# Kernel tuning notes

Hardware: AMD Instinct MI355X
Metric: run time of the kernel (lower is better)

## Reference

```python
import jax, jax.numpy as jnp
from jax import lax
import numpy as np

N_QUBITS = 8


def _apply_1q(state, w, n, m00, m01, m10, m11):
    # state: (B, 2, 2, ..., 2); wire w lives on axis 1+w (wire 0 = most significant)
    st = jnp.moveaxis(state, 1 + w, -1)
    a0, a1 = st[..., 0], st[..., 1]
    b0 = m00 * a0 + m01 * a1
    b1 = m10 * a0 + m11 * a1
    st = jnp.stack([b0, b1], axis=-1)
    return jnp.moveaxis(st, -1, 1 + w)


def _apply_rx(state, theta, w, n):
    # RX(t) = [[cos t/2, -i sin t/2], [-i sin t/2, cos t/2]], per-batch theta
    shp = (-1,) + (1,) * (n - 1)
    c = jnp.cos(theta / 2).reshape(shp).astype(jnp.complex64)
    s = (-1j) * jnp.sin(theta / 2).reshape(shp).astype(jnp.complex64)
    return _apply_1q(state, w, n, c, s, s, c)


def _apply_rz(state, theta, w, n):
    # RZ(t) = diag(e^{-it/2}, e^{+it/2})
    shp = (-1,) + (1,) * (n - 1)
    e = jnp.exp(-0.5j * theta.astype(jnp.complex64)).reshape(shp)
    return _apply_1q(state, w, n, e, jnp.zeros_like(e), jnp.zeros_like(e), jnp.conj(e))


def _apply_cnot(state, ctrl, tgt, n):
    st = jnp.moveaxis(state, (1 + ctrl, 1 + tgt), (-2, -1))
    st = jnp.stack([st[..., 0, :], st[..., 1, ::-1]], axis=-2)
    return jnp.moveaxis(st, (-2, -1), (1 + ctrl, 1 + tgt))


def _circuit_probs(params):
    # params: (B, n). Simulate the fixed PennyLane circuit: for each wire w:
    # RX(params[w]) on w, RZ(params[(w+1)%n]) on w, CNOT(w, (w+1)%n).
    B, n = params.shape
    state = jnp.zeros((B, 2 ** n), jnp.complex64).at[:, 0].set(1.0)
    state = state.reshape((B,) + (2,) * n)
    for w in range(n):
        state = _apply_rx(state, params[:, w], w, n)
        state = _apply_rz(state, params[:, (w + 1) % n], w, n)
        state = _apply_cnot(state, w, (w + 1) % n, n)
    probs = jnp.abs(state.reshape(B, -1)) ** 2  # (B, 2^n), wire 0 most significant
    p = probs[:, :n]
    return p / jnp.sum(p, axis=1, keepdims=True)


def _qgate(W, b, x):
    params = x @ W.T + b  # (B, n_qubits)
    return _circuit_probs(params)


def setup_inputs() -> dict:
    key = jax.random.key(0)
    ks = jax.random.split(key, 9)
    S, B, D, N = 1024, 128, 256, N_QUBITS
    fan_in = D + N
    lim = 1.0 / np.sqrt(fan_in)
    u = lambda k, shape: jax.random.uniform(k, shape, jnp.float32, -lim, lim)
    return {
        "inputs": jax.random.normal(ks[0], (S, B, D), jnp.float32),
        "Wf": u(ks[1], (N, fan_in)), "bf": u(ks[2], (N,)),
        "Wi": u(ks[3], (N, fan_in)), "bi": u(ks[4], (N,)),
        "Wu": u(ks[5], (N, fan_in)), "bu": u(ks[6], (N,)),
        "Wo": u(ks[7], (N, fan_in)), "bo": u(ks[8], (N,)),
    }


def reference(inputs, Wf, bf, Wi, bi, Wu, bu, Wo, bo):
    S, B, D = inputs.shape
    N = Wf.shape[0]  # hidden_dim == n_qubits
    h0 = jnp.zeros((B, N), inputs.dtype)
    c0 = jnp.zeros((B, N), inputs.dtype)

    def step(carry, x):
        h, c = carry
        comb = jnp.concatenate([x, h], axis=1)  # (B, D+N)
        f = _qgate(Wf, bf, comb)
        i = _qgate(Wi, bi, comb)
        g = jnp.tanh(_qgate(Wu, bu, comb))
        o = _qgate(Wo, bo, comb)
        c_new = f * c + i * g
        h_new = o * jnp.tanh(c_new)
        return (h_new, c_new), h_new

    (h_n, c_n), outputs = lax.scan(step, (h0, c0), inputs)
    return outputs, h_n, c_n
```

## Files before the change

kernel.cpp:

```cpp
#include <hip/hip_runtime.h>

#define S_STEPS 1024
#define BATCH 128
#define NQ 8
#define XW_FLOATS (BATCH * 32 * 1024)

using v2f     = float __attribute__((ext_vector_type(2)));
using frag_ab = __attribute__((ext_vector_type(8))) short;
using frag_cd = __attribute__((ext_vector_type(4))) float;

#define INV2PI 0.15915494309189535f

template<int CTRL>
__device__ __forceinline__ float dppf(float x) {
  return __int_as_float(__builtin_amdgcn_update_dpp(0, __float_as_int(x), CTRL, 0xf, 0xf, true));
}
__device__ __forceinline__ float bperm(int addr, float v) {
  return __int_as_float(__builtin_amdgcn_ds_bpermute(addr, __float_as_int(v)));
}
__device__ __forceinline__ short f2bf(float f) {
  unsigned u = __float_as_uint(f);
  return (short)((u + 0x7FFFu + ((u >> 16) & 1u)) >> 16);
}
__device__ __forceinline__ float bf2f(short h) {
  return __uint_as_float(((unsigned)(unsigned short)h) << 16);
}

__global__ __launch_bounds__(512) void qlstm_pre(
    const float* __restrict__ x,
    const float* __restrict__ Wf, const float* __restrict__ bf_,
    const float* __restrict__ Wi, const float* __restrict__ bi,
    const float* __restrict__ Wu, const float* __restrict__ bu,
    const float* __restrict__ Wo, const float* __restrict__ bo,
    float* __restrict__ xw)
{
  __shared__ short whi[32 * 264];
  __shared__ short wlo[32 * 264];

  const int tid = threadIdx.x;

  {
    const int base = tid * 16;
    const int c = base >> 8, k0 = base & 255;
    const int g = c >> 3, w = c & 7;
    const float* Wg = (g == 0) ? Wf : (g == 1) ? Wi : (g == 2) ? Wu : Wo;
    const float* p = Wg + w * 264 + k0;
    const int o = c * 264 + k0;
#pragma unroll
    for (int q = 0; q < 2; ++q) {
      float4 va = *(const float4*)(p + q * 8);
      float4 vb = *(const float4*)(p + q * 8 + 4);
      float vv[8] = {va.x, va.y, va.z, va.w, vb.x, vb.y, vb.z, vb.w};
      frag_ab h8, l8;
#pragma unroll
      for (int j = 0; j < 8; ++j) {
        float wv = vv[j] * INV2PI;
        short h = f2bf(wv);
        h8[j] = h;
        l8[j] = f2bf(wv - bf2f(h));
      }
      *(frag_ab*)&whi[o + q * 8] = h8;
      *(frag_ab*)&wlo[o + q * 8] = l8;
    }
  }
  __syncthreads();

  const int lane = tid & 63;
  const int m  = lane & 15;
  const int kg = lane >> 4;
  const int gid = blockIdx.x * 8 + (tid >> 6);
  const int b  = gid >> 6;
  const int t0 = (gid & 63) << 4;

  float bb[2][4];
#pragma unroll
  for (int n = 0; n < 2; ++n)
#pragma unroll
    for (int r = 0; r < 4; ++r) {
      int c = n * 16 + kg * 4 + r;
      int g = c >> 3, w = c & 7;
      const float* bg = (g == 0) ? bf_ : (g == 1) ? bi : (g == 2) ? bu : bo;
      bb[n][r] = bg[w] * INV2PI;
    }

  const float* xbase = x + ((size_t)(t0 + m) * 128 + b) * 256 + kg * 8;
  const int w0 = m * 264 + kg * 8;
  const int w1 = w0 + 16 * 264;

  frag_cd acc0 = {0.f, 0.f, 0.f, 0.f};
  frag_cd acc1 = {0.f, 0.f, 0.f, 0.f};

  float4 xv0 = *(const float4*)(xbase);
  float4 xv1 = *(const float4*)(xbase + 4);

#pragma unroll 1
  for (int kk = 0; kk < 8; ++kk) {
    float4 nx0 = xv0, nx1 = xv1;
    if (kk < 7) {
      nx0 = *(const float4*)(xbase + (kk + 1) * 32);
      nx1 = *(const float4*)(xbase + (kk + 1) * 32 + 4);
    }
    frag_ab a0h = *(const frag_ab*)&whi[w0 + kk * 32];
    frag_ab a0l = *(const frag_ab*)&wlo[w0 + kk * 32];
    frag_ab a1h = *(const frag_ab*)&whi[w1 + kk * 32];
    frag_ab a1l = *(const frag_ab*)&wlo[w1 + kk * 32];

    float xf[8] = {xv0.x, xv0.y, xv0.z, xv0.w, xv1.x, xv1.y, xv1.z, xv1.w};
    frag_ab xh, xl;
#pragma unroll
    for (int j = 0; j < 8; ++j) {
      short h = f2bf(xf[j]);
      xh[j] = h;
      xl[j] = f2bf(xf[j] - bf2f(h));
    }

    acc0 = __builtin_amdgcn_mfma_f32_16x16x32_bf16(a0h, xh, acc0, 0, 0, 0);
    acc0 = __builtin_amdgcn_mfma_f32_16x16x32_bf16(a0l, xh, acc0, 0, 0, 0);
    acc0 = __builtin_amdgcn_mfma_f32_16x16x32_bf16(a0h, xl, acc0, 0, 0, 0);
    acc1 = __builtin_amdgcn_mfma_f32_16x16x32_bf16(a1h, xh, acc1, 0, 0, 0);
    acc1 = __builtin_amdgcn_mfma_f32_16x16x32_bf16(a1l, xh, acc1, 0, 0, 0);
    acc1 = __builtin_amdgcn_mfma_f32_16x16x32_bf16(a1h, xl, acc1, 0, 0, 0);

    xv0 = nx0; xv1 = nx1;
  }

#pragma unroll
  for (int n = 0; n < 2; ++n) {
    const frag_cd a = n ? acc1 : acc0;
#pragma unroll
    for (int r = 0; r < 4; ++r)
      xw[((size_t)(b * 32 + n * 16 + kg * 4 + r)) * 1024 + t0 + m] = a[r] + bb[n][r];
  }
}

__global__ __launch_bounds__(64) void qlstm_seq(
    const float* __restrict__ xw,
    const float* __restrict__ Wf, const float* __restrict__ Wi,
    const float* __restrict__ Wu, const float* __restrict__ Wo,
    float* __restrict__ out)
{
  const int lane = threadIdx.x;
  const int r = lane & 15, g = r >> 2, k = r & 3;
  const int b = blockIdx.x * 4 + (lane >> 4);
  const int B6 = (k >> 1) & 1, B7 = k & 1;
  const bool isB7 = (B7 != 0);
  const float s6 = B6 ? -1.f : 1.f,        o6 = B6 ? 1.f : 0.f;
  const float s7 = (B7^B6) ? -1.f : 1.f,   o7 = (B7^B6) ? 1.f : 0.f;
  const int wA = (k == 0) ? 0 : (k == 1) ? 5 : 7;
  const int wB = (k == 0) ? 1 : (k == 1) ? 6 : 7;

  const float* Wg = (g == 0) ? Wf : (g == 1) ? Wi : (g == 2) ? Wu : Wo;
  v2f whA2[4], whB2[4];
#pragma unroll
  for (int j2 = 0; j2 < 4; ++j2) {
    whA2[j2] = (v2f){Wg[wA*264+256+2*j2] * INV2PI, Wg[wA*264+256+2*j2+1] * INV2PI};
    whB2[j2] = (v2f){Wg[wB*264+256+2*j2] * INV2PI, Wg[wB*264+256+2*j2+1] * INV2PI};
  }

  const int aF = (((lane & 48) | k) << 2);
  const int aI = aF + 16, aU = aF + 32, aO = aF + 48;

  v2f h2[4];
#pragma unroll
  for (int j = 0; j < 4; ++j) h2[j] = (v2f){0.f, 0.f};
  float cA = 0.f, cB = 0.f, hqA = 0.f, hqB = 0.f;

  const float* bxw = xw + (size_t)b * 32768;
  const float4* pA = (const float4*)(bxw + (size_t)(g * 8 + wA) * 1024);
  const float4* pB = (const float4*)(bxw + (size_t)(g * 8 + wB) * 1024);
  float4 curA = pA[0], nxtA = pA[1];
  float4 curB = pB[0], nxtB = pB[1];

  const int soff = b * 8 + r;
  float houtS[16];

#pragma unroll 1
  for (int Tb = 0; Tb < S_STEPS; Tb += 16) {
#pragma unroll
    for (int sg = 0; sg < 4; ++sg) {
      int gi = (Tb >> 2) + sg;
      int tp = gi + 2; tp = (tp > 255) ? 255 : tp;
      float4 nnA = pA[tp], nnB = pB[tp];
#pragma unroll
      for (int u = 0; u < 4; ++u) {
        float xa = (u==0)?curA.x:(u==1)?curA.y:(u==2)?curA.z:curA.w;
        float xb = (u==0)?curB.x:(u==1)?curB.y:(u==2)?curB.z:curB.w;
        v2f accA = whA2[0]*h2[0]; accA = whA2[1]*h2[1] + accA;
        accA = whA2[2]*h2[2] + accA; accA = whA2[3]*h2[3] + accA;
        v2f accB = whB2[0]*h2[0]; accB = whB2[1]*h2[1] + accB;
        accB = whB2[2]*h2[2] + accB; accB = whB2[3]*h2[3] + accB;
        float pa = (xa + accA.x) + accA.y;
        float pb = (xb + accB.x) + accB.y;
        float ccA = fmaf(0.5f, __builtin_amdgcn_cosf(pa), 0.5f);
        float ccB = fmaf(0.5f, __builtin_amdgcn_cosf(pb), 0.5f);

        float C0 = dppf<0x00>(ccA), C1 = dppf<0x00>(ccB);
        float C5 = dppf<0x55>(ccA), C6 = dppf<0x55>(ccB);
        float C7 = dppf<0xAA>(ccA);

        float S0v = 1.f - C0, S1v = 1.f - C1;
        float P01 = C0 * C1, Q01 = S0v * S1v;
        float sel01 = isB7 ? Q01 : P01;
        float F7  = fmaf(s7, C7, o7);
        float F6A = fmaf(s6, C6, o6);
        float e7  = sel01 * F7;
        float dA  = C5 * F6A;
        float dB  = (1.f + dA) - (C5 + F6A);
        float d56 = C5 * C6;
        float U0  = fmaf(2.f, d56, 1.f - (C5 + C6));
        float S7v = 1.f - C7;
        float T0  = fmaf(fmaf(2.f, C7, -1.f), U0, S7v);
        float sden = fmaf(P01 - Q01, T0, Q01);
        float es  = e7 * __builtin_amdgcn_rcpf(sden);
        float pnA = es * dA, pnB = es * dB;

        float fvA = bperm(aF, pnA), ivA = bperm(aI, pnA);
        float uvA = bperm(aU, pnA), ovA = bperm(aO, pnA);
        float fvB = bperm(aF, pnB), ivB = bperm(aI, pnB);
        float uvB = bperm(aU, pnB), ovB = bperm(aO, pnB);

        float t2A = uvA * uvA;
        float gvA = uvA * (t2A + 15.f) * __builtin_amdgcn_rcpf(fmaf(6.f, t2A, 15.f));
        cA = fmaf(fvA, cA, ivA * gvA);
        float eA = __builtin_amdgcn_exp2f(fminf(cA, 15.f) * 2.88539008f);
        hqA = ovA * fmaf(-2.f, __builtin_amdgcn_rcpf(eA + 1.f), 1.f);
        float t2B = uvB * uvB;
        float gvB = uvB * (t2B + 15.f) * __builtin_amdgcn_rcpf(fmaf(6.f, t2B, 15.f));
        cB = fmaf(fvB, cB, ivB * gvB);
        float eB = __builtin_amdgcn_exp2f(fminf(cB, 15.f) * 2.88539008f);
        hqB = ovB * fmaf(-2.f, __builtin_amdgcn_rcpf(eB + 1.f), 1.f);

        h2[0].x = dppf<0x00>(hqA); h2[0].y = dppf<0x55>(hqA);
        h2[1].x = dppf<0xAA>(hqA); h2[1].y = dppf<0xFF>(hqA);
        h2[2].x = dppf<0x00>(hqB); h2[2].y = dppf<0x55>(hqB);
        h2[3].x = dppf<0xAA>(hqB); h2[3].y = dppf<0xFF>(hqB);

        houtS[sg * 4 + u] = (g == 0) ? hqA : hqB;
      }
      curA = nxtA; nxtA = nnA;
      curB = nxtB; nxtB = nnB;
    }
    if (r < 8) {
      float* op = out + (size_t)Tb * (BATCH * NQ) + soff;
#pragma unroll
      for (int tt = 0; tt < 16; ++tt)
        op[(size_t)tt * (BATCH * NQ)] = houtS[tt];
    }
  }
  if (r < 8) {
    size_t o1 = (size_t)S_STEPS * BATCH * NQ + soff;
    out[o1] = (g == 0) ? hqA : hqB;
    out[o1 + (size_t)BATCH * NQ] = (g == 0) ? cA : cB;
  }
}

extern "C" void kernel_launch(void* const* d_in, const int* in_sizes, int n_in,
                              void* d_out, int out_size, void* d_ws, size_t ws_size,
                              hipStream_t stream) {
  const float* x  = (const float*)d_in[0];
  const float* Wf = (const float*)d_in[1];
  const float* bf = (const float*)d_in[2];
  const float* Wi = (const float*)d_in[3];
  const float* bi = (const float*)d_in[4];
  const float* Wu = (const float*)d_in[5];
  const float* bu = (const float*)d_in[6];
  const float* Wo = (const float*)d_in[7];
  const float* bo = (const float*)d_in[8];
  float* xw  = (float*)d_ws;
  float* out = (float*)d_out;

  qlstm_pre<<<1024, 512, 0, stream>>>(x, Wf, bf, Wi, bi, Wu, bu, Wo, bo, xw);
  qlstm_seq<<<32, 64, 0, stream>>>(xw, Wf, Wi, Wu, Wo, out);
}
```

Baseline: 447.4 us.

## Split input projection K across waves and replace bpermute gate gather with DPP

The input-projection kernel now launches one block per (batch, 16-step tile). It stages x rows in swizzled shared memory, gives each of the 8 waves one 32-wide K slice with register-resident split-bf16 weights, and reduces the partial MFMA results through shared memory. This removes the per-wave K loop and the shared-memory weight staging, in exchange for 8x more blocks and an extra LDS reduction. In the sequential recurrence kernel, the eight ds_bpermute lane gathers of gate values are replaced with DPP row shuffles plus selects. The aim is to shorten the latency-critical step chain.

Result: no change. 452.5 us (+1.1%).

```diff
diff --git a/kernel.cpp b/kernel.cpp
--- a/kernel.cpp
+++ b/kernel.cpp
@@ -3,7 +3,6 @@
 #define S_STEPS 1024
 #define BATCH 128
 #define NQ 8
-#define XW_FLOATS (BATCH * 32 * 1024)
 
 using v2f     = float __attribute__((ext_vector_type(2)));
 using frag_ab = __attribute__((ext_vector_type(8))) short;
@@ -14,9 +13,6 @@
 template<int CTRL>
 __device__ __forceinline__ float dppf(float x) {
   return __int_as_float(__builtin_amdgcn_update_dpp(0, __float_as_int(x), CTRL, 0xf, 0xf, true));
-}
-__device__ __forceinline__ float bperm(int addr, float v) {
-  return __int_as_float(__builtin_amdgcn_ds_bpermute(addr, __float_as_int(v)));
 }
 __device__ __forceinline__ short f2bf(float f) {
   unsigned u = __float_as_uint(f);
@@ -34,102 +30,85 @@
     const float* __restrict__ Wo, const float* __restrict__ bo,
     float* __restrict__ xw)
 {
-  __shared__ short whi[32 * 264];
-  __shared__ short wlo[32 * 264];
-
-  const int tid = threadIdx.x;
+  __shared__ float xbuf[16 * 256];
+  __shared__ float red[8 * 520];
+
+  const int tid  = threadIdx.x;
+  const int lane = tid & 63;
+  const int wid  = tid >> 6;
+  const int b    = blockIdx.x >> 6;
+  const int t0   = (blockIdx.x & 63) << 4;
 
   {
-    const int base = tid * 16;
-    const int c = base >> 8, k0 = base & 255;
+    const int r = tid >> 5, s = tid & 31;
+    const float* xrow = x + ((size_t)(t0 + r) * 128 + b) * 256;
+    float4 f0 = *(const float4*)(xrow + s * 4);
+    float4 f1 = *(const float4*)(xrow + 128 + s * 4);
+    *(float4*)&xbuf[r * 256 + 4 * ((s)      ^ (r & 7))] = f0;
+    *(float4*)&xbuf[r * 256 + 4 * ((32 + s) ^ (r & 7))] = f1;
+  }
+
+  const int m  = lane & 15;
+  const int kg = lane >> 4;
+  frag_ab awh[2], awl[2];
+#pragma unroll
+  for (int n = 0; n < 2; ++n) {
+    const int c = n * 16 + m;
     const int g = c >> 3, w = c & 7;
     const float* Wg = (g == 0) ? Wf : (g == 1) ? Wi : (g == 2) ? Wu : Wo;
-    const float* p = Wg + w * 264 + k0;
-    const int o = c * 264 + k0;
-#pragma unroll
-    for (int q = 0; q < 2; ++q) {
-      float4 va = *(const float4*)(p + q * 8);
-      float4 vb = *(const float4*)(p + q * 8 + 4);
-      float vv[8] = {va.x, va.y, va.z, va.w, vb.x, vb.y, vb.z, vb.w};
-      frag_ab h8, l8;
-#pragma unroll
-      for (int j = 0; j < 8; ++j) {
-        float wv = vv[j] * INV2PI;
-        short h = f2bf(wv);
-        h8[j] = h;
-        l8[j] = f2bf(wv - bf2f(h));
-      }
-      *(frag_ab*)&whi[o + q * 8] = h8;
-      *(frag_ab*)&wlo[o + q * 8] = l8;
+    const float* p = Wg + w * 264 + wid * 32 + kg * 8;
+    float4 a  = *(const float4*)(p);
+    float4 bq = *(const float4*)(p + 4);
+    float vv[8] = {a.x, a.y, a.z, a.w, bq.x, bq.y, bq.z, bq.w};
+#pragma unroll
+    for (int j = 0; j < 8; ++j) {
+      float wv = vv[j] * INV2PI;
+      short h = f2bf(wv);
+      awh[n][j] = h;
+      awl[n][j] = f2bf(wv - bf2f(h));
     }
   }
+
   __syncthreads();
 
-  const int lane = tid & 63;
-  const int m  = lane & 15;
-  const int kg = lane >> 4;
-  const int gid = blockIdx.x * 8 + (tid >> 6);
-  const int b  = gid >> 6;
-  const int t0 = (gid & 63) << 4;
-
-  float bb[2][4];
-#pragma unroll
-  for (int n = 0; n < 2; ++n)
-#pragma unroll
-    for (int r = 0; r < 4; ++r) {
-      int c = n * 16 + kg * 4 + r;
-      int g = c >> 3, w = c & 7;
-      const float* bg = (g == 0) ? bf_ : (g == 1) ? bi : (g == 2) ? bu : bo;
-      bb[n][r] = bg[w] * INV2PI;
-    }
-
-  const float* xbase = x + ((size_t)(t0 + m) * 128 + b) * 256 + kg * 8;
-  const int w0 = m * 264 + kg * 8;
-  const int w1 = w0 + 16 * 264;
+  float4 v0 = *(const float4*)&xbuf[m * 256 + 4 * ((wid * 8 + kg * 2)     ^ (m & 7))];
+  float4 v1 = *(const float4*)&xbuf[m * 256 + 4 * ((wid * 8 + kg * 2 + 1) ^ (m & 7))];
+  float xf[8] = {v0.x, v0.y, v0.z, v0.w, v1.x, v1.y, v1.z, v1.w};
+  frag_ab xh, xl;
+#pragma unroll
+  for (int j = 0; j < 8; ++j) {
+    short h = f2bf(xf[j]);
+    xh[j] = h;
+    xl[j] = f2bf(xf[j] - bf2f(h));
+  }
 
   frag_cd acc0 = {0.f, 0.f, 0.f, 0.f};
   frag_cd acc1 = {0.f, 0.f, 0.f, 0.f};
-
-  float4 xv0 = *(const float4*)(xbase);
-  float4 xv1 = *(const float4*)(xbase + 4);
-
-#pragma unroll 1
-  for (int kk = 0; kk < 8; ++kk) {
-    float4 nx0 = xv0, nx1 = xv1;
-    if (kk < 7) {
-      nx0 = *(const float4*)(xbase + (kk + 1) * 32);
-      nx1 = *(const float4*)(xbase + (kk + 1) * 32 + 4);
-    }
-    frag_ab a0h = *(const frag_ab*)&whi[w0 + kk * 32];
-    frag_ab a0l = *(const frag_ab*)&wlo[w0 + kk * 32];
-    frag_ab a1h = *(const frag_ab*)&whi[w1 + kk * 32];
-    frag_ab a1l = *(const frag_ab*)&wlo[w1 + kk * 32];
-
-    float xf[8] = {xv0.x, xv0.y, xv0.z, xv0.w, xv1.x, xv1.y, xv1.z, xv1.w};
-    frag_ab xh, xl;
-#pragma unroll
-    for (int j = 0; j < 8; ++j) {
-      short h = f2bf(xf[j]);
-      xh[j] = h;
-      xl[j] = f2bf(xf[j] - bf2f(h));
-    }
-
-    acc0 = __builtin_amdgcn_mfma_f32_16x16x32_bf16(a0h, xh, acc0, 0, 0, 0);
-    acc0 = __builtin_amdgcn_mfma_f32_16x16x32_bf16(a0l, xh, acc0, 0, 0, 0);
-    acc0 = __builtin_amdgcn_mfma_f32_16x16x32_bf16(a0h, xl, acc0, 0, 0, 0);
-    acc1 = __builtin_amdgcn_mfma_f32_16x16x32_bf16(a1h, xh, acc1, 0, 0, 0);
-    acc1 = __builtin_amdgcn_mfma_f32_16x16x32_bf16(a1l, xh, acc1, 0, 0, 0);
-    acc1 = __builtin_amdgcn_mfma_f32_16x16x32_bf16(a1h, xl, acc1, 0, 0, 0);
-
-    xv0 = nx0; xv1 = nx1;
-  }
-
-#pragma unroll
-  for (int n = 0; n < 2; ++n) {
-    const frag_cd a = n ? acc1 : acc0;
-#pragma unroll
-    for (int r = 0; r < 4; ++r)
-      xw[((size_t)(b * 32 + n * 16 + kg * 4 + r)) * 1024 + t0 + m] = a[r] + bb[n][r];
+  acc0 = __builtin_amdgcn_mfma_f32_16x16x32_bf16(awh[0], xh, acc0, 0, 0, 0);
+  acc0 = __builtin_amdgcn_mfma_f32_16x16x32_bf16(awl[0], xh, acc0, 0, 0, 0);
+  acc0 = __builtin_amdgcn_mfma_f32_16x16x32_bf16(awh[0], xl, acc0, 0, 0, 0);
+  acc1 = __builtin_amdgcn_mfma_f32_16x16x32_bf16(awh[1], xh, acc1, 0, 0, 0);
+  acc1 = __builtin_amdgcn_mfma_f32_16x16x32_bf16(awl[1], xh, acc1, 0, 0, 0);
+  acc1 = __builtin_amdgcn_mfma_f32_16x16x32_bf16(awh[1], xl, acc1, 0, 0, 0);
+
+#pragma unroll
+  for (int rho = 0; rho < 4; ++rho) {
+    red[(rho)     * 520 + wid * 64 + lane] = acc0[rho];
+    red[(4 + rho) * 520 + wid * 64 + lane] = acc1[rho];
+  }
+  __syncthreads();
+
+  {
+    const int c  = tid >> 4, mm = tid & 15;
+    const int v  = ((c >> 4) << 2) | (c & 3);
+    const int lp = (((c >> 2) & 3) << 4) | mm;
+    float sum = 0.f;
+#pragma unroll
+    for (int w8 = 0; w8 < 8; ++w8)
+      sum += red[v * 520 + w8 * 64 + lp];
+    const int g = c >> 3, w = c & 7;
+    const float* bg = (g == 0) ? bf_ : (g == 1) ? bi : (g == 2) ? bu : bo;
+    xw[((size_t)(b * 32 + c)) * 1024 + t0 + mm] = sum + bg[w] * INV2PI;
   }
 }
 
@@ -148,6 +127,8 @@
   const float s7 = (B7^B6) ? -1.f : 1.f,   o7 = (B7^B6) ? 1.f : 0.f;
   const int wA = (k == 0) ? 0 : (k == 1) ? 5 : 7;
   const int wB = (k == 0) ? 1 : (k == 1) ? 6 : 7;
+  const bool g0 = (g & 1) != 0;
+  const bool g1 = (g & 2) != 0;
 
   const float* Wg = (g == 0) ? Wf : (g == 1) ? Wi : (g == 2) ? Wu : Wo;
   v2f whA2[4], whB2[4];
@@ -156,9 +137,6 @@
     whA2[j2] = (v2f){Wg[wA*264+256+2*j2] * INV2PI, Wg[wA*264+256+2*j2+1] * INV2PI};
     whB2[j2] = (v2f){Wg[wB*264+256+2*j2] * INV2PI, Wg[wB*264+256+2*j2+1] * INV2PI};
   }
-
-  const int aF = (((lane & 48) | k) << 2);
-  const int aI = aF + 16, aU = aF + 32, aO = aF + 48;
 
   v2f h2[4];
 #pragma unroll
@@ -214,10 +192,29 @@
         float es  = e7 * __builtin_amdgcn_rcpf(sden);
         float pnA = es * dA, pnB = es * dB;
 
-        float fvA = bperm(aF, pnA), ivA = bperm(aI, pnA);
-        float uvA = bperm(aU, pnA), ovA = bperm(aO, pnA);
-        float fvB = bperm(aF, pnB), ivB = bperm(aI, pnB);
-        float uvB = bperm(aU, pnB), ovB = bperm(aO, pnB);
+        float rMA = dppf<0x140>(pnA);
+        float rHA = dppf<0x141>(pnA);
+        float r1A = dppf<0x1B>(rHA);
+        float r3A = dppf<0x1B>(rMA);
+        float r2A = dppf<0x141>(rMA);
+        float rMB = dppf<0x140>(pnB);
+        float rHB = dppf<0x141>(pnB);
+        float r1B = dppf<0x1B>(rHB);
+        float r3B = dppf<0x1B>(rMB);
+        float r2B = dppf<0x141>(rMB);
+
+        float s32A = g0 ? r3A : r2A;  float s10A = g0 ? r1A : pnA;
+        float sv1A = g0 ? pnA : r1A;  float s23A = g0 ? r2A : r3A;
+        float fvA = g1 ? s32A : s10A;
+        float uvA = g1 ? s10A : s32A;
+        float ivA = g1 ? s23A : sv1A;
+        float ovA = g1 ? sv1A : s23A;
+        float s32B = g0 ? r3B : r2B;  float s10B = g0 ? r1B : pnB;
+        float sv1B = g0 ? pnB : r1B;  float s23B = g0 ? r2B : r3B;
+        float fvB = g1 ? s32B : s10B;
+        float uvB = g1 ? s10B : s32B;
+        float ivB = g1 ? s23B : sv1B;
+        float ovB = g1 ? sv1B : s23B;
 
         float t2A = uvA * uvA;
         float gvA = uvA * (t2A + 15.f) * __builtin_amdgcn_rcpf(fmaf(6.f, t2A, 15.f));
@@ -269,6 +266,6 @@
   float* xw  = (float*)d_ws;
   float* out = (float*)d_out;
 
-  qlstm_pre<<<1024, 512, 0, stream>>>(x, Wf, bf, Wi, bi, Wu, bu, Wo, bo, xw);
+  qlstm_pre<<<8192, 512, 0, stream>>>(x, Wf, bf, Wi, bi, Wu, bu, Wo, bo, xw);
   qlstm_seq<<<32, 64, 0, stream>>>(xw, Wf, Wi, Wu, Wo, out);
 }
```
